# Kernel tuning notes

Measured on AMD Instinct MI355X. Metric: run time of the kernel, lower is better.

Reference implementation:

```python
import jax, jax.numpy as jnp
import numpy as np

T = 256          # n_tokens
APR = 3          # atoms_per_residue
N = T * APR      # n_atoms = 768
CA = 128         # atom_embedding_size
CP = 16          # atom_pair_embedding_size
CT = 384         # token_embedding_size
CS = 384         # single_embedding_size
CZ = 128         # pair_embedding_size
NB = 3           # num_block
H = 4            # num_head
DH = CA // H
NQ = 32          # num_queries (query block size)
NK = 128         # num_keys (local key window)


def _ln(x, g, b):
    m = jnp.mean(x, -1, keepdims=True)
    v = jnp.mean((x - m) ** 2, -1, keepdims=True)
    return (x - m) * jax.lax.rsqrt(v + 1e-5) * g + b


def setup_inputs() -> dict:
    key = jax.random.key(0)
    ks = jax.random.split(key, 32)
    w = lambda k, shape: jax.random.normal(k, shape, jnp.float32) * 0.02
    return {
        "ref_pos": jax.random.normal(ks[0], (N, 3), jnp.float32),
        "ref_space_uid": jax.random.randint(ks[1], (N,), 0, T),
        "r": jax.random.normal(ks[2], (N, 3), jnp.float32),
        "s": jax.random.normal(ks[3], (T, CS), jnp.float32),
        "z": jax.random.normal(ks[4], (T, T, CZ), jnp.float32),
        "W_pos": w(ks[5], (3, CA)),
        "W_pos_offset": w(ks[6], (3, CP)),
        "W_inv_sq_dist": w(ks[7], (1, CP)),
        "W_mask": w(ks[8], (1, CP)),
        "W_cond_a": w(ks[9], (CA, CP)),
        "W_cond_b": w(ks[10], (CA, CP)),
        "ln_s_g": jnp.ones((CS,), jnp.float32), "ln_s_b": jnp.zeros((CS,), jnp.float32),
        "W_single": w(ks[11], (CS, CA)),
        "ln_z_g": jnp.ones((CZ,), jnp.float32), "ln_z_b": jnp.zeros((CZ,), jnp.float32),
        "W_pair": w(ks[12], (CZ, CP)),
        "W_noisy": w(ks[13], (3, CA)),
        "W_mlp1": w(ks[14], (CP, CP)),
        "W_mlp2": w(ks[15], (CP, CP)),
        "W_mlp3": w(ks[16], (CP, CP)),
        "at_ln_g": jnp.ones((NB, CA), jnp.float32), "at_ln_b": jnp.zeros((NB, CA), jnp.float32),
        "at_Wq": w(ks[17], (NB, CA, CA)),
        "at_Wk": w(ks[18], (NB, CA, CA)),
        "at_Wv": w(ks[19], (NB, CA, CA)),
        "at_Wg": w(ks[20], (NB, CA, CA)),
        "at_lnp_g": jnp.ones((NB, CP), jnp.float32), "at_lnp_b": jnp.zeros((NB, CP), jnp.float32),
        "at_Wb": w(ks[21], (NB, CP, H)),
        "at_Wo": w(ks[22], (NB, CA, CA)),
        "at_ln2_g": jnp.ones((NB, CA), jnp.float32), "at_ln2_b": jnp.zeros((NB, CA), jnp.float32),
        "at_Wt1": w(ks[23], (NB, CA, 4 * CA)),
        "at_Wt2": w(ks[24], (NB, 4 * CA, CA)),
        "W_proj": w(ks[25], (CA, CT)),
    }


def _forward(ref_pos, ref_space_uid, r, s, z, W_pos, W_pos_offset, W_inv_sq_dist, W_mask,
             W_cond_a, W_cond_b, ln_s_g, ln_s_b, W_single, ln_z_g, ln_z_b, W_pair, W_noisy,
             W_mlp1, W_mlp2, W_mlp3, at_ln_g, at_ln_b, at_Wq, at_Wk, at_Wv, at_Wg,
             at_lnp_g, at_lnp_b, at_Wb, at_Wo, at_ln2_g, at_ln2_b, at_Wt1, at_Wt2, W_proj):
    c = ref_pos @ W_pos                                             # [N,CA]
    dist = ref_pos[:, None, :] - ref_pos[None, :, :]                # [N,N,3]
    maskf = (ref_space_uid[:, None] == ref_space_uid[None, :])[..., None].astype(jnp.float32)
    pair = (dist @ W_pos_offset) * maskf                            # [N,N,CP]
    sq = jnp.sum(dist * dist, -1, keepdims=True)                    # [N,N,1]
    pair = pair + ((1.0 / (1.0 + sq)) @ W_inv_sq_dist) * maskf
    pair = pair + (maskf @ W_mask) * maskf
    q = c
    # r is not None branch
    c = c + _ln(jnp.tile(s, (APR, 1)), ln_s_g, ln_s_b) @ W_single
    pair = pair + _ln(jnp.tile(z, (APR, APR, 1)), ln_z_g, ln_z_b) @ W_pair
    q = q + r @ W_noisy
    rc = jax.nn.relu(c)
    pair = pair + (rc @ W_cond_a)[:, None, :] + (rc @ W_cond_b)[None, :, :]
    h = jax.nn.relu(pair) @ W_mlp1
    h = jax.nn.relu(h) @ W_mlp2
    h = jax.nn.relu(h) @ W_mlp3
    pair = pair + h
    # sequence-local attention mask (AF3-style: query blocks of NQ attend a NK-wide window)
    idx = jnp.arange(N)
    center = (idx // NQ) * NQ + (NQ - 1) / 2.0
    beta = jnp.where(jnp.abs(idx[None, :].astype(jnp.float32) - center[:, None]) < NK / 2.0, 0.0, -1e9)
    scale = 1.0 / np.sqrt(DH).astype(np.float32)
    x = q
    for b in range(NB):
        a = _ln(x, at_ln_g[b], at_ln_b[b])
        qh = (a @ at_Wq[b]).reshape(N, H, DH)
        kh = (a @ at_Wk[b]).reshape(N, H, DH)
        vh = (a @ at_Wv[b]).reshape(N, H, DH)
        bias = _ln(pair, at_lnp_g[b], at_lnp_b[b]) @ at_Wb[b]       # [N,N,H]
        logits = jnp.einsum('ihd,jhd->hij', qh, kh) * scale + bias.transpose(2, 0, 1) + beta[None]
        attn = jax.nn.softmax(logits, axis=-1)
        o = jnp.einsum('hij,jhd->ihd', attn, vh)
        g = jax.nn.sigmoid(a @ at_Wg[b]).reshape(N, H, DH)
        x = x + (o * g).reshape(N, CA) @ at_Wo[b]
        t = _ln(x, at_ln2_g[b], at_ln2_b[b])
        x = x + jax.nn.relu(t @ at_Wt1[b]) @ at_Wt2[b]
    qout = jax.nn.relu(x @ W_proj)                                  # [N,CT]
    a_out = jnp.mean(qout.reshape(T, APR, CT), axis=-2)             # [T,CT]
    return a_out, qout, c, pair


def reference(ref_pos, ref_space_uid, r, s, z, W_pos, W_pos_offset, W_inv_sq_dist, W_mask,
              W_cond_a, W_cond_b, ln_s_g, ln_s_b, W_single, ln_z_g, ln_z_b, W_pair, W_noisy,
              W_mlp1, W_mlp2, W_mlp3, at_ln_g, at_ln_b, at_Wq, at_Wk, at_Wv, at_Wg,
              at_lnp_g, at_lnp_b, at_Wb, at_Wo, at_ln2_g, at_ln2_b, at_Wt1, at_Wt2, W_proj):
    return _forward(ref_pos, ref_space_uid, r, s, z, W_pos, W_pos_offset, W_inv_sq_dist, W_mask,
                    W_cond_a, W_cond_b, ln_s_g, ln_s_b, W_single, ln_z_g, ln_z_b, W_pair, W_noisy,
                    W_mlp1, W_mlp2, W_mlp3, at_ln_g, at_ln_b, at_Wq, at_Wk, at_Wv, at_Wg,
                    at_lnp_g, at_lnp_b, at_Wb, at_Wo, at_ln2_g, at_ln2_b, at_Wt1, at_Wt2, W_proj)
```

## Files before the change

kernel.cpp:

```cpp
#include <hip/hip_runtime.h>
#include <math.h>


__device__ __forceinline__ float sigmoidf_(float v) { return 1.f / (1.f + __expf(-v)); }

typedef __attribute__((ext_vector_type(4))) short s16x4;
typedef __attribute__((ext_vector_type(8))) short s16x8;
typedef __attribute__((ext_vector_type(4))) float f32x4;

__device__ __forceinline__ unsigned bfpack(float a, float b) {
  return (__float_as_uint(a) >> 16) | (__float_as_uint(b) & 0xFFFF0000u);
}
__device__ __forceinline__ short bf1(float a) { return (short)(__float_as_uint(a) >> 16); }

__global__ __launch_bounds__(256) void k_front(
    const float* __restrict__ z, const float* __restrict__ zg,
    const float* __restrict__ zlb, const float* __restrict__ W_pair,
    float* __restrict__ zp,
    const float* __restrict__ s, const float* __restrict__ g,
    const float* __restrict__ b, const float* __restrict__ W_single,
    const float* __restrict__ ref_pos, const float* __restrict__ r,
    const float* __restrict__ W_pos, const float* __restrict__ W_noisy,
    const float* __restrict__ Wca, const float* __restrict__ Wcb,
    float* __restrict__ c_out, float* __restrict__ x,
    float* __restrict__ ca, float* __restrict__ cb) {
  __shared__ __align__(128) float sm[5392];
  int t = threadIdx.x;
  int bid = blockIdx.x;
  if (bid < 1024) {
    float* bcp = sm + 5120;
    float* Bc = sm + 5376;
    {
      int ch = t & 15, kseg = t >> 4;
      float a = 0.f;
#pragma unroll
      for (int e = 0; e < 8; e++) {
        int k = kseg * 8 + e;
        a += zlb[k] * W_pair[k * 16 + ch];
      }
      bcp[kseg * 16 + ch] = a;
    }
    __syncthreads();
    if (t < 16) {
      float a = 0.f;
#pragma unroll
      for (int kseg = 0; kseg < 16; kseg++) a += bcp[kseg * 16 + t];
      Bc[t] = a;
    }
    __syncthreads();
    int w = t >> 6, l = t & 63;
    int kb = l & 15, rg = l >> 4;
    int row0 = bid * 64 + w * 16;
    char* stgw = (char*)(sm + w * 1280);
    float4 za[4], zb[4];
    float m_[4], rs_[4];
#pragma unroll
    for (int rr = 0; rr < 4; rr++) {
      long base = (long)(row0 + rg * 4 + rr) * 128 + kb * 8;
      za[rr] = *(const float4*)&z[base];
      zb[rr] = *(const float4*)&z[base + 4];
      float ps = za[rr].x + za[rr].y + za[rr].z + za[rr].w +
                 zb[rr].x + zb[rr].y + zb[rr].z + zb[rr].w;
      float pq = za[rr].x * za[rr].x + za[rr].y * za[rr].y + za[rr].z * za[rr].z +
                 za[rr].w * za[rr].w + zb[rr].x * zb[rr].x + zb[rr].y * zb[rr].y +
                 zb[rr].z * zb[rr].z + zb[rr].w * zb[rr].w;
#pragma unroll
      for (int o = 1; o < 16; o <<= 1) { ps += __shfl_xor(ps, o); pq += __shfl_xor(pq, o); }
      m_[rr] = ps * (1.f / 128.f);
      rs_[rr] = rsqrtf(pq * (1.f / 128.f) - m_[rr] * m_[rr] + 1e-5f);
    }
    {
      int kc = kb >> 1;
      int cbase = (kb & 1) * 8;
#pragma unroll
      for (int e = 0; e < 8; e++) {
        float a0 = ((e < 4 ? (&za[0].x)[e] : (&zb[0].x)[e - 4]) - m_[0]) * rs_[0];
        float a1 = ((e < 4 ? (&za[1].x)[e] : (&zb[1].x)[e - 4]) - m_[1]) * rs_[1];
        float a2 = ((e < 4 ? (&za[2].x)[e] : (&zb[2].x)[e - 4]) - m_[2]) * rs_[2];
        float a3 = ((e < 4 ? (&za[3].x)[e] : (&zb[3].x)[e - 4]) - m_[3]) * rs_[3];
        char* wp = stgw + kc * 640 + (cbase + e) * 32 + rg * 8;
        *(uint2*)wp = make_uint2(bfpack(a0, a1), bfpack(a2, a3));
      }
    }
    int c = l & 15;
    s16x8 bw[8];
#pragma unroll
    for (int kc = 0; kc < 8; kc++) {
      short e0, e1, e2, e3;
      {
        int kk = kc * 16 + 4 * rg;
        e0 = bf1(zg[kk] * W_pair[kk * 16 + c]);
        e1 = bf1(zg[kk + 1] * W_pair[(kk + 1) * 16 + c]);
        e2 = bf1(zg[kk + 2] * W_pair[(kk + 2) * 16 + c]);
        e3 = bf1(zg[kk + 3] * W_pair[(kk + 3) * 16 + c]);
      }
      bw[kc] = s16x8{e0, e1, e2, e3, (short)0, (short)0, (short)0, (short)0};
    }
    unsigned sbase = (unsigned)(uintptr_t)stgw;
    f32x4 acc = {0.f, 0.f, 0.f, 0.f};
#pragma unroll
    for (int kc = 0; kc < 8; kc++) {
      unsigned ra = sbase + (unsigned)(kc * 640 + c * 8 + rg * 128);
      s16x4 tr;
      asm volatile("s_waitcnt lgkmcnt(0)\n\tds_read_b64_tr_b16 %0, %1\n\ts_waitcnt lgkmcnt(0)"
                   : "=v"(tr) : "v"(ra) : "memory");
      s16x8 a8 = {tr[0], tr[1], tr[2], tr[3], (short)0, (short)0, (short)0, (short)0};
      acc = __builtin_amdgcn_mfma_f32_16x16x32_bf16(a8, bw[kc], acc, 0, 0, 0);
    }
    float bc = Bc[c];
#pragma unroll
    for (int rr = 0; rr < 4; rr++) {
      int row = row0 + rg * 4 + rr;
      zp[(long)row * 16 + c] = acc[rr] + bc;
    }
  } else {
    int tok = bid - 1024;
    float* sln = sm;
    float* ws = sm + 384;
    float* red = sm + 4480;
    float* rc = sm + 4488;
    float v0 = 0.f, v1 = 0.f, v2 = 0.f;
    if (t < 128) {
      v0 = s[tok * 384 + t]; v1 = s[tok * 384 + 128 + t]; v2 = s[tok * 384 + 256 + t];
      float ps = v0 + v1 + v2, pq = v0 * v0 + v1 * v1 + v2 * v2;
#pragma unroll
      for (int o = 1; o < 64; o <<= 1) { ps += __shfl_xor(ps, o); pq += __shfl_xor(pq, o); }
      if ((t & 63) == 0) { red[t >> 6] = ps; red[2 + (t >> 6)] = pq; }
    }
    __syncthreads();
    float ctv = 0.f;
    if (t < 128) {
      float mean = (red[0] + red[1]) * (1.f / 384.f);
      float var = (red[2] + red[3]) * (1.f / 384.f) - mean * mean;
      float rstd = rsqrtf(var + 1e-5f);
      sln[t] = (v0 - mean) * rstd * g[t] + b[t];
      sln[128 + t] = (v1 - mean) * rstd * g[128 + t] + b[128 + t];
      sln[256 + t] = (v2 - mean) * rstd * g[256 + t] + b[256 + t];
    }
    for (int c0 = 0; c0 < 384; c0 += 32) {
      __syncthreads();
#pragma unroll
      for (int m = 0; m < 4; m++) {
        int idx = (t + 256 * m) * 4;
        *(float4*)&ws[idx] = *(const float4*)&W_single[c0 * 128 + idx];
      }
      __syncthreads();
      if (t < 128) {
#pragma unroll 8
        for (int kk = 0; kk < 32; kk++) ctv += sln[c0 + kk] * ws[kk * 128 + t];
      }
    }
    float wp0 = 0.f, wp1 = 0.f, wp2 = 0.f, wn0 = 0.f, wn1 = 0.f, wn2 = 0.f;
    if (t < 128) {
      wp0 = W_pos[t]; wp1 = W_pos[128 + t]; wp2 = W_pos[256 + t];
      wn0 = W_noisy[t]; wn1 = W_noisy[128 + t]; wn2 = W_noisy[256 + t];
    }
#pragma unroll
    for (int a = 0; a < 3; a++) {
      int i = tok + 256 * a;
      float cc = 0.f;
      if (t < 128) {
        float p0 = ref_pos[i * 3], p1 = ref_pos[i * 3 + 1], p2 = ref_pos[i * 3 + 2];
        float r0 = r[i * 3], r1 = r[i * 3 + 1], r2 = r[i * 3 + 2];
        float c0 = p0 * wp0 + p1 * wp1 + p2 * wp2;
        x[i * 128 + t] = c0 + r0 * wn0 + r1 * wn1 + r2 * wn2;
        cc = c0 + ctv;
        c_out[i * 128 + t] = cc;
      }
      __syncthreads();
      if (t < 128) rc[t] = fmaxf(cc, 0.f);
      __syncthreads();
      if (t < 128) {
        int out_id = t >> 2, q = t & 3;
        const float* Wm = (out_id < 16) ? Wca : Wcb;
        int ch = out_id & 15;
        float acc = 0.f;
#pragma unroll
        for (int kk = 0; kk < 32; kk++) { int k = q * 32 + kk; acc += rc[k] * Wm[k * 16 + ch]; }
        acc += __shfl_xor(acc, 1);
        acc += __shfl_xor(acc, 2);
        if (q == 0) { if (out_id < 16) ca[i * 16 + ch] = acc; else cb[i * 16 + ch] = acc; }
      }
    }
  }
}

__global__ __launch_bounds__(256) void k_pairq(
    const float* __restrict__ ref_pos, const int* __restrict__ uid,
    const float* __restrict__ Wpo, const float* __restrict__ Wisd,
    const float* __restrict__ Wmask, const float* __restrict__ W1,
    const float* __restrict__ W2, const float* __restrict__ W3,
    const float* __restrict__ zp, const float* __restrict__ ca,
    const float* __restrict__ cb, const float* __restrict__ lnp_g,
    const float* __restrict__ lnp_b, const float* __restrict__ Wb,
    float* __restrict__ pair_out, float* __restrict__ biasA,
    const float* __restrict__ x, const float* __restrict__ lng,
    const float* __restrict__ lnb, const float* __restrict__ Wq,
    const float* __restrict__ Wk, const float* __restrict__ Wv,
    const float* __restrict__ Wg, float* __restrict__ qkvg) {
  __shared__ float jsx[256], jsy[256], jsz[256];
  __shared__ int jsu[256];
  __shared__ __align__(128) short stg[4][1280];
  __shared__ __align__(16) float pfs[4][1056];
  __shared__ float wgb[192];
  __shared__ float kbs[12];
  int t = threadIdx.x;
  int bid = blockIdx.x;
  if (bid >= 2304) {
    int r0 = (bid - 2304) * 2;
    float* asr_ = jsx;
    float* red_ = jsy;
    int row = t >> 7, c = t & 127;
    float xv = x[(r0 + row) * 128 + c];
    {
      float ps = xv, pq = xv * xv;
#pragma unroll
      for (int o = 1; o < 64; o <<= 1) { ps += __shfl_xor(ps, o); pq += __shfl_xor(pq, o); }
      int wv = t >> 6;
      if ((t & 63) == 0) { red_[wv] = ps; red_[4 + wv] = pq; }
      __syncthreads();
      float mean = (red_[2 * row] + red_[2 * row + 1]) * (1.f / 128.f);
      float var = (red_[4 + 2 * row] + red_[4 + 2 * row + 1]) * (1.f / 128.f) - mean * mean;
      float rstd = rsqrtf(var + 1e-5f);
      asr_[row * 128 + c] = (xv - mean) * rstd * lng[c] + lnb[c];
    }
    __syncthreads();
    {
      int c4 = (t & 127) * 4, row2 = t >> 7;
      int mtx = c4 >> 7, lc = c4 & 127;
      const float* Wm = (mtx == 0) ? Wq : (mtx == 1) ? Wk : (mtx == 2) ? Wv : Wg;
      float a0 = 0.f, a1 = 0.f, a2 = 0.f, a3 = 0.f;
#pragma unroll 8
      for (int k = 0; k < 128; k++) {
        float4 w = *(const float4*)&Wm[k * 128 + lc];
        float av = asr_[row2 * 128 + k];
        a0 += av * w.x; a1 += av * w.y; a2 += av * w.z; a3 += av * w.w;
      }
      *(float4*)&qkvg[(r0 + row2) * 512 + c4] = make_float4(a0, a1, a2, a3);
    }
    return;
  }
  int i = bid / 3, jb = bid % 3;
  int jg = jb * 256 + t;
  jsx[t] = ref_pos[jg * 3];
  jsy[t] = ref_pos[jg * 3 + 1];
  jsz[t] = ref_pos[jg * 3 + 2];
  jsu[t] = uid[jg];
  if (t >= 64) {
    int e = t - 64;
    if (e < 192) {
      int bq = e >> 6, k = (e >> 2) & 15, h = e & 3;
      wgb[e] = lnp_g[bq * 16 + k] * Wb[bq * 64 + k * 4 + h];
    }
  }
  if (t >= 48 && t < 60) {
    int e = t - 48, bq = e >> 2, h = e & 3;
    float a = 0.f;
#pragma unroll
    for (int cc = 0; cc < 16; cc++) a += lnp_b[bq * 16 + cc] * Wb[bq * 64 + cc * 4 + h];
    kbs[e] = a;
  }
  int w = t >> 6, l = t & 63;
  int c = l & 15, gr = l >> 4;
  float pix = ref_pos[i * 3], piy = ref_pos[i * 3 + 1], piz = ref_pos[i * 3 + 2];
  int ui = uid[i];
  float w0c = Wpo[c], w1c = Wpo[16 + c], w2c = Wpo[32 + c];
  float wic = Wisd[c], wmc = Wmask[c], cac = ca[i * 16 + c];
  s16x8 bw0 = {bf1(W1[(4 * gr + 0) * 16 + c]), bf1(W1[(4 * gr + 1) * 16 + c]),
               bf1(W1[(4 * gr + 2) * 16 + c]), bf1(W1[(4 * gr + 3) * 16 + c]),
               (short)0, (short)0, (short)0, (short)0};
  s16x8 bw1 = {bf1(W2[(4 * gr + 0) * 16 + c]), bf1(W2[(4 * gr + 1) * 16 + c]),
               bf1(W2[(4 * gr + 2) * 16 + c]), bf1(W2[(4 * gr + 3) * 16 + c]),
               (short)0, (short)0, (short)0, (short)0};
  s16x8 bw2 = {bf1(W3[(4 * gr + 0) * 16 + c]), bf1(W3[(4 * gr + 1) * 16 + c]),
               bf1(W3[(4 * gr + 2) * 16 + c]), bf1(W3[(4 * gr + 3) * 16 + c]),
               (short)0, (short)0, (short)0, (short)0};
  __syncthreads();
  char* sb = (char*)&stg[w][0];
  unsigned sbase = (unsigned)(uintptr_t)sb;
  f32x4 z4 = {0.f, 0.f, 0.f, 0.f};
#pragma unroll
  for (int g = 0; g < 4; g++) {
    float p0_, p1_, p2_, p3_;
    {
      int jl0 = w * 64 + g * 16 + 4 * gr;
#pragma unroll
      for (int r = 0; r < 4; r++) {
        int jloc = jl0 + r;
        int j = jb * 256 + jloc;
        float d0 = pix - jsx[jloc], d1 = piy - jsy[jloc], d2 = piz - jsz[jloc];
        float mk = (ui == jsu[jloc]) ? 1.f : 0.f;
        float inv = 1.f / (1.f + d0 * d0 + d1 * d1 + d2 * d2);
        float zv = zp[((long)((i & 255) << 8) + jloc) * 16 + c];
        float cbv = cb[j * 16 + c];
        float pv = mk * (d0 * w0c + d1 * w1c + d2 * w2c + inv * wic + wmc) + zv + cbv + cac;
        if (r == 0) p0_ = pv; else if (r == 1) p1_ = pv; else if (r == 2) p2_ = pv; else p3_ = pv;
      }
    }
    char* wp = sb + g * 640 + c * 32 + gr * 8;
    unsigned ra = sbase + (unsigned)(g * 640 + c * 8 + gr * 128);
    *(uint2*)wp = make_uint2(bfpack(fmaxf(p0_, 0.f), fmaxf(p1_, 0.f)),
                             bfpack(fmaxf(p2_, 0.f), fmaxf(p3_, 0.f)));
    s16x4 tr0;
    asm volatile("s_waitcnt lgkmcnt(0)\n\tds_read_b64_tr_b16 %0, %1\n\ts_waitcnt lgkmcnt(0)"
                 : "=v"(tr0) : "v"(ra) : "memory");
    s16x8 a8 = {tr0[0], tr0[1], tr0[2], tr0[3], (short)0, (short)0, (short)0, (short)0};
    f32x4 h1 = __builtin_amdgcn_mfma_f32_16x16x32_bf16(a8, bw0, z4, 0, 0, 0);
    *(uint2*)wp = make_uint2(bfpack(fmaxf(h1[0], 0.f), fmaxf(h1[1], 0.f)),
                             bfpack(fmaxf(h1[2], 0.f), fmaxf(h1[3], 0.f)));
    s16x4 tr1;
    asm volatile("s_waitcnt lgkmcnt(0)\n\tds_read_b64_tr_b16 %0, %1\n\ts_waitcnt lgkmcnt(0)"
                 : "=v"(tr1) : "v"(ra) : "memory");
    s16x8 a8b = {tr1[0], tr1[1], tr1[2], tr1[3], (short)0, (short)0, (short)0, (short)0};
    f32x4 h2 = __builtin_amdgcn_mfma_f32_16x16x32_bf16(a8b, bw1, z4, 0, 0, 0);
    *(uint2*)wp = make_uint2(bfpack(fmaxf(h2[0], 0.f), fmaxf(h2[1], 0.f)),
                             bfpack(fmaxf(h2[2], 0.f), fmaxf(h2[3], 0.f)));
    s16x4 tr2;
    asm volatile("s_waitcnt lgkmcnt(0)\n\tds_read_b64_tr_b16 %0, %1\n\ts_waitcnt lgkmcnt(0)"
                 : "=v"(tr2) : "v"(ra) : "memory");
    s16x8 a8c = {tr2[0], tr2[1], tr2[2], tr2[3], (short)0, (short)0, (short)0, (short)0};
    f32x4 h3 = __builtin_amdgcn_mfma_f32_16x16x32_bf16(a8c, bw2, z4, 0, 0, 0);
    float f0 = p0_ + h3[0], f1 = p1_ + h3[1], f2 = p2_ + h3[2], f3 = p3_ + h3[3];
    {
      int jl0 = w * 64 + g * 16 + 4 * gr;
      long pb = ((long)i * 768 + (long)(jb * 256 + jl0)) * 16 + c;
      pair_out[pb] = f0;
      pair_out[pb + 16] = f1;
      pair_out[pb + 32] = f2;
      pair_out[pb + 48] = f3;
    }
    *(float4*)&pfs[w][g * 264 + c * 16 + 4 * gr] = make_float4(f0, f1, f2, f3);
  }
  asm volatile("s_waitcnt lgkmcnt(0)" ::: "memory");
  int qb = i >> 5;
  int j = jb * 256 + t;
  unsigned jw = (unsigned)(j - (qb * 32 - 48));
  if (jw < 128u) {
    int gt = (t >> 4) & 3, jr = t & 15;
    float v[16];
#pragma unroll
    for (int cc = 0; cc < 16; cc++) v[cc] = pfs[w][gt * 264 + cc * 16 + jr];
    float m = 0.f;
#pragma unroll
    for (int cc = 0; cc < 16; cc++) m += v[cc];
    m *= (1.f / 16.f);
    float vv = 0.f;
#pragma unroll
    for (int cc = 0; cc < 16; cc++) { float d = v[cc] - m; vv += d * d; }
    float rs = rsqrtf(vv * (1.f / 16.f) + 1e-5f);
    float nrm[16];
#pragma unroll
    for (int cc = 0; cc < 16; cc++) nrm[cc] = (v[cc] - m) * rs;
    int qi = i & 31;
#pragma unroll
    for (int bq = 0; bq < 3; bq++) {
      float o0 = kbs[bq * 4 + 0], o1 = kbs[bq * 4 + 1];
      float o2 = kbs[bq * 4 + 2], o3 = kbs[bq * 4 + 3];
#pragma unroll
      for (int k = 0; k < 16; k++) {
        float nv = nrm[k];
        float4 wv = *(float4*)&wgb[bq * 64 + k * 4];
        o0 += nv * wv.x; o1 += nv * wv.y; o2 += nv * wv.z; o3 += nv * wv.w;
      }
      long base = (long)(bq * 96 + qb * 4) * 4096 + (long)qi * 128 + jw;
      biasA[base] = o0;
      biasA[base + 4096] = o1;
      biasA[base + 2 * 4096] = o2;
      biasA[base + 3 * 4096] = o3;
    }
  }
}

__global__ __launch_bounds__(256) void k_attn2(
    const float* __restrict__ qkvg, const float* __restrict__ biasb,
    float* __restrict__ og) {
  int qt = blockIdx.x >> 2, h = blockIdx.x & 3, t = threadIdx.x;
  int i0 = qt * 16;
  int qb32 = qt >> 1;
  int lo = qb32 * 32 - 48;
  int qoff = (qt & 1) * 16;
  __shared__ float qs[16][36];
  __shared__ float ks[128][36];
  __shared__ float vs[128][36];
  __shared__ float L[16][132];
  {
    int e = t * 8;
    int qi = e >> 7, k8 = e & 127;
    const float* bb = &biasb[(long)(qb32 * 4 + h) * 4096 + (long)(qoff + qi) * 128];
#pragma unroll
    for (int m = 0; m < 2; m++) {
      int k4 = k8 + m * 4;
      int j4 = lo + k4;
      float4 bv;
      if (j4 >= 0 && j4 <= 764) bv = *(const float4*)&bb[k4];
      else bv = make_float4(-1e30f, -1e30f, -1e30f, -1e30f);
      *(float4*)&L[qi][k4] = bv;
    }
  }
  if (t < 128) {
    int qi = t >> 3, dq = (t & 7) * 4;
    *(float4*)&qs[qi][dq] = *(const float4*)&qkvg[(i0 + qi) * 512 + h * 32 + dq];
  }
  {
    int kj = t >> 1, dh = (t & 1) * 16;
    int j = lo + kj;
    if (j >= 0 && j < 768) {
      const float4* sk = (const float4*)&qkvg[j * 512 + 128 + h * 32 + dh];
      const float4* sv = (const float4*)&qkvg[j * 512 + 256 + h * 32 + dh];
#pragma unroll
      for (int m = 0; m < 4; m++) {
        *(float4*)&ks[kj][dh + 4 * m] = sk[m];
        *(float4*)&vs[kj][dh + 4 * m] = sv[m];
      }
    } else {
      float4 zz = {0, 0, 0, 0};
#pragma unroll
      for (int m = 0; m < 4; m++) {
        *(float4*)&ks[kj][dh + 4 * m] = zz;
        *(float4*)&vs[kj][dh + 4 * m] = zz;
      }
    }
  }
  __syncthreads();
  const float scale = 0.17677669529663687f;
  {
    int qi = t & 15, kb = t >> 4;
    float4 qr[8];
#pragma unroll
    for (int m = 0; m < 8; m++) qr[m] = *(float4*)&qs[qi][m * 4];
#pragma unroll
    for (int kk = 0; kk < 8; kk++) {
      int kj = kb * 8 + kk;
      float acc = 0.f;
#pragma unroll
      for (int m = 0; m < 8; m++) {
        float4 kv = *(float4*)&ks[kj][m * 4];
        acc += qr[m].x * kv.x + qr[m].y * kv.y + qr[m].z * kv.z + qr[m].w * kv.w;
      }
      L[qi][kj] += acc * scale;
    }
  }
  __syncthreads();
  int qi = t >> 4, sg = t & 15;
  float mx = -1e30f;
#pragma unroll
  for (int k2 = 0; k2 < 8; k2++) mx = fmaxf(mx, L[qi][sg * 8 + k2]);
#pragma unroll
  for (int o = 1; o < 16; o <<= 1) mx = fmaxf(mx, __shfl_xor(mx, o));
  float sum = 0.f;
#pragma unroll
  for (int k2 = 0; k2 < 8; k2++) {
    int kj = sg * 8 + k2;
    float e = __expf(L[qi][kj] - mx);
    L[qi][kj] = e;
    sum += e;
  }
#pragma unroll
  for (int o = 1; o < 16; o <<= 1) sum += __shfl_xor(sum, o);
  float rden = 1.f / sum;
  __syncthreads();
  {
    int d2 = (t & 15) * 2;
    float a0 = 0.f, a1 = 0.f;
#pragma unroll 8
    for (int kj = 0; kj < 128; kj++) {
      float p = L[qi][kj];
      float2 v = *(float2*)&vs[kj][d2];
      a0 += p * v.x; a1 += p * v.y;
    }
    int i = i0 + qi;
    float2 gr = *(const float2*)&qkvg[i * 512 + 384 + h * 32 + d2];
    float2 o2;
    o2.x = a0 * rden * sigmoidf_(gr.x);
    o2.y = a1 * rden * sigmoidf_(gr.y);
    *(float2*)&og[i * 128 + h * 32 + d2] = o2;
  }
}

template <int MODE>
__global__ __launch_bounds__(512, 1) void k_fusedT(
    const float* __restrict__ og, const float* __restrict__ Wo,
    const float* __restrict__ g2, const float* __restrict__ b2,
    const float* __restrict__ Wt1, const float* __restrict__ Wt2,
    float* __restrict__ x,
    const float* __restrict__ lng_n, const float* __restrict__ lnb_n,
    const float* __restrict__ Wq, const float* __restrict__ Wk,
    const float* __restrict__ Wv, const float* __restrict__ Wg,
    float* __restrict__ qkvg, const float* __restrict__ W_proj,
    float* __restrict__ out) {
  int t = threadIdx.x;
  int r0 = blockIdx.x * 3;
  __shared__ float osr[3][128];
  __shared__ float xns[3][128];
  __shared__ float asr[3][128];
  __shared__ float hs[3][512];
  __shared__ float part[4][3][128];
  __shared__ float part2[4][3][512];
  __shared__ float red[12];
  if (t < 384) {
    int rr = t >> 7, c = t & 127;
    osr[rr][c] = og[(r0 + rr) * 128 + c];
    xns[rr][c] = x[(r0 + rr) * 128 + c];
  }
  __syncthreads();
  if (t < 384) {
    int c4 = (t & 31) * 4, row = (t >> 5) % 3, q = t / 96;
    int k0 = q * 32;
    float a0 = 0.f, a1 = 0.f, a2 = 0.f, a3 = 0.f;
#pragma unroll 8
    for (int kk = 0; kk < 32; kk++) {
      int k = k0 + kk;
      float4 w = *(const float4*)&Wo[k * 128 + c4];
      float av = osr[row][k];
      a0 += av * w.x; a1 += av * w.y; a2 += av * w.z; a3 += av * w.w;
    }
    *(float4*)&part[q][row][c4] = make_float4(a0, a1, a2, a3);
  }
  __syncthreads();
  if (t < 384) {
    int rr = t >> 7, c = t & 127;
    float xv = xns[rr][c] + part[0][rr][c] + part[1][rr][c] + part[2][rr][c] + part[3][rr][c];
    float ps = xv, pq = xv * xv;
#pragma unroll
    for (int o = 1; o < 64; o <<= 1) { ps += __shfl_xor(ps, o); pq += __shfl_xor(pq, o); }
    int wv = t >> 6;
    if ((t & 63) == 0) { red[wv] = ps; red[6 + wv] = pq; }
  }
  __syncthreads();
  if (t < 384) {
    int rr = t >> 7, c = t & 127;
    float xv = xns[rr][c] + part[0][rr][c] + part[1][rr][c] + part[2][rr][c] + part[3][rr][c];
    float mean = (red[2 * rr] + red[2 * rr + 1]) * (1.f / 128.f);
    float var = (red[6 + 2 * rr] + red[6 + 2 * rr + 1]) * (1.f / 128.f) - mean * mean;
    float rstd = rsqrtf(var + 1e-5f);
    xns[rr][c] = xv;
    asr[rr][c] = (xv - mean) * rstd * g2[c] + b2[c];
  }
  __syncthreads();
  {
    int cg4 = (t & 127) * 4, ks = t >> 7;
    int k0 = ks * 32;
    float a00 = 0.f, a01 = 0.f, a02 = 0.f, a03 = 0.f;
    float a10 = 0.f, a11 = 0.f, a12 = 0.f, a13 = 0.f;
    float a20 = 0.f, a21 = 0.f, a22 = 0.f, a23 = 0.f;
#pragma unroll 8
    for (int kk = 0; kk < 32; kk++) {
      int k = k0 + kk;
      float4 w = *(const float4*)&Wt1[k * 512 + cg4];
      float v0 = asr[0][k], v1 = asr[1][k], v2 = asr[2][k];
      a00 += v0 * w.x; a01 += v0 * w.y; a02 += v0 * w.z; a03 += v0 * w.w;
      a10 += v1 * w.x; a11 += v1 * w.y; a12 += v1 * w.z; a13 += v1 * w.w;
      a20 += v2 * w.x; a21 += v2 * w.y; a22 += v2 * w.z; a23 += v2 * w.w;
    }
    *(float4*)&part2[ks][0][cg4] = make_float4(a00, a01, a02, a03);
    *(float4*)&part2[ks][1][cg4] = make_float4(a10, a11, a12, a13);
    *(float4*)&part2[ks][2][cg4] = make_float4(a20, a21, a22, a23);
  }
  __syncthreads();
  {
#pragma unroll
    for (int row = 0; row < 3; row++) {
      float v = part2[0][row][t] + part2[1][row][t] + part2[2][row][t] + part2[3][row][t];
      hs[row][t] = fmaxf(v, 0.f);
    }
  }
  __syncthreads();
  {
    int cg4 = (t & 31) * 4, ks = t >> 5;
    int k0 = ks * 32;
    float a00 = 0.f, a01 = 0.f, a02 = 0.f, a03 = 0.f;
    float a10 = 0.f, a11 = 0.f, a12 = 0.f, a13 = 0.f;
    float a20 = 0.f, a21 = 0.f, a22 = 0.f, a23 = 0.f;
#pragma unroll 8
    for (int kk = 0; kk < 32; kk++) {
      int k = k0 + kk;
      float4 w = *(const float4*)&Wt2[k * 128 + cg4];
      float v0 = hs[0][k], v1 = hs[1][k], v2 = hs[2][k];
      a00 += v0 * w.x; a01 += v0 * w.y; a02 += v0 * w.z; a03 += v0 * w.w;
      a10 += v1 * w.x; a11 += v1 * w.y; a12 += v1 * w.z; a13 += v1 * w.w;
      a20 += v2 * w.x; a21 += v2 * w.y; a22 += v2 * w.z; a23 += v2 * w.w;
    }
    float* p3 = &part2[0][0][0];
    *(float4*)&p3[(ks * 3 + 0) * 128 + cg4] = make_float4(a00, a01, a02, a03);
    *(float4*)&p3[(ks * 3 + 1) * 128 + cg4] = make_float4(a10, a11, a12, a13);
    *(float4*)&p3[(ks * 3 + 2) * 128 + cg4] = make_float4(a20, a21, a22, a23);
  }
  __syncthreads();
  if (t < 384) {
    int rr = t >> 7, c = t & 127;
    const float* p3 = &part2[0][0][0];
    float acc = 0.f;
#pragma unroll
    for (int ks = 0; ks < 16; ks++) acc += p3[(ks * 3 + rr) * 128 + c];
    float xf = xns[rr][c] + acc;
    x[(r0 + rr) * 128 + c] = xf;
    xns[rr][c] = xf;
  }
  __syncthreads();
  if (MODE == 1) {
    if (t < 384) {
      int rr = t >> 7, c = t & 127;
      float xv = xns[rr][c];
      float ps = xv, pq = xv * xv;
#pragma unroll
      for (int o = 1; o < 64; o <<= 1) { ps += __shfl_xor(ps, o); pq += __shfl_xor(pq, o); }
      int wv = t >> 6;
      if ((t & 63) == 0) { red[wv] = ps; red[6 + wv] = pq; }
    }
    __syncthreads();
    if (t < 384) {
      int rr = t >> 7, c = t & 127;
      float xv = xns[rr][c];
      float mean = (red[2 * rr] + red[2 * rr + 1]) * (1.f / 128.f);
      float var = (red[6 + 2 * rr] + red[6 + 2 * rr + 1]) * (1.f / 128.f) - mean * mean;
      float rstd = rsqrtf(var + 1e-5f);
      asr[rr][c] = (xv - mean) * rstd * lng_n[c] + lnb_n[c];
    }
    __syncthreads();
    {
      int cg4 = (t & 127) * 4, ks = t >> 7;
      int k0 = ks * 32;
      int mtx = cg4 >> 7, lc = cg4 & 127;
      const float* Wm = (mtx == 0) ? Wq : (mtx == 1) ? Wk : (mtx == 2) ? Wv : Wg;
      float a00 = 0.f, a01 = 0.f, a02 = 0.f, a03 = 0.f;
      float a10 = 0.f, a11 = 0.f, a12 = 0.f, a13 = 0.f;
      float a20 = 0.f, a21 = 0.f, a22 = 0.f, a23 = 0.f;
#pragma unroll 8
      for (int kk = 0; kk < 32; kk++) {
        int k = k0 + kk;
        float4 w = *(const float4*)&Wm[k * 128 + lc];
        float v0 = asr[0][k], v1 = asr[1][k], v2 = asr[2][k];
        a00 += v0 * w.x; a01 += v0 * w.y; a02 += v0 * w.z; a03 += v0 * w.w;
        a10 += v1 * w.x; a11 += v1 * w.y; a12 += v1 * w.z; a13 += v1 * w.w;
        a20 += v2 * w.x; a21 += v2 * w.y; a22 += v2 * w.z; a23 += v2 * w.w;
      }
      *(float4*)&part2[ks][0][cg4] = make_float4(a00, a01, a02, a03);
      *(float4*)&part2[ks][1][cg4] = make_float4(a10, a11, a12, a13);
      *(float4*)&part2[ks][2][cg4] = make_float4(a20, a21, a22, a23);
    }
    __syncthreads();
    {
#pragma unroll
      for (int row = 0; row < 3; row++) {
        float v = part2[0][row][t] + part2[1][row][t] + part2[2][row][t] + part2[3][row][t];
        qkvg[(r0 + row) * 512 + t] = v;
      }
    }
  }
  if (MODE == 2) {
    if (t < 384) {
      int tk = blockIdx.x;
      float a0 = 0.f, a1 = 0.f, a2 = 0.f;
#pragma unroll 8
      for (int k = 0; k < 128; k++) {
        float w = W_proj[k * 384 + t];
        a0 += xns[0][k] * w; a1 += xns[1][k] * w; a2 += xns[2][k] * w;
      }
      a0 = fmaxf(a0, 0.f); a1 = fmaxf(a1, 0.f); a2 = fmaxf(a2, 0.f);
      out[98304 + (tk * 3 + 0) * 384 + t] = a0;
      out[98304 + (tk * 3 + 1) * 384 + t] = a1;
      out[98304 + (tk * 3 + 2) * 384 + t] = a2;
      out[tk * 384 + t] = (a0 + a1 + a2) * (1.f / 3.f);
    }
  }
}

extern "C" void kernel_launch(void* const* d_in, const int* in_sizes, int n_in,
                              void* d_out, int out_size, void* d_ws, size_t ws_size,
                              hipStream_t stream) {
  const float* ref_pos  = (const float*)d_in[0];
  const int*   uid      = (const int*)d_in[1];
  const float* r        = (const float*)d_in[2];
  const float* s        = (const float*)d_in[3];
  const float* z        = (const float*)d_in[4];
  const float* W_pos    = (const float*)d_in[5];
  const float* Wpo      = (const float*)d_in[6];
  const float* Wisd     = (const float*)d_in[7];
  const float* Wmask    = (const float*)d_in[8];
  const float* Wca      = (const float*)d_in[9];
  const float* Wcb      = (const float*)d_in[10];
  const float* ln_s_g   = (const float*)d_in[11];
  const float* ln_s_b   = (const float*)d_in[12];
  const float* W_single = (const float*)d_in[13];
  const float* ln_z_g   = (const float*)d_in[14];
  const float* ln_z_b   = (const float*)d_in[15];
  const float* W_pair   = (const float*)d_in[16];
  const float* W_noisy  = (const float*)d_in[17];
  const float* W_mlp1   = (const float*)d_in[18];
  const float* W_mlp2   = (const float*)d_in[19];
  const float* W_mlp3   = (const float*)d_in[20];
  const float* at_ln_g  = (const float*)d_in[21];
  const float* at_ln_b  = (const float*)d_in[22];
  const float* at_Wq    = (const float*)d_in[23];
  const float* at_Wk    = (const float*)d_in[24];
  const float* at_Wv    = (const float*)d_in[25];
  const float* at_Wg    = (const float*)d_in[26];
  const float* at_lnp_g = (const float*)d_in[27];
  const float* at_lnp_b = (const float*)d_in[28];
  const float* at_Wb    = (const float*)d_in[29];
  const float* at_Wo    = (const float*)d_in[30];
  const float* at_ln2_g = (const float*)d_in[31];
  const float* at_ln2_b = (const float*)d_in[32];
  const float* at_Wt1   = (const float*)d_in[33];
  const float* at_Wt2   = (const float*)d_in[34];
  const float* W_proj   = (const float*)d_in[35];
  float* out = (float*)d_out;
  float* W = (float*)d_ws;
  float* x     = W;
  float* ca    = W + 98304;
  float* cb    = W + 110592;
  float* zp    = W + 122880;
  float* biasA = W + 1171456;
  float* qkvg  = W + 2351104;
  float* og    = W + 2744320;

  k_front<<<1280, 256, 0, stream>>>(z, ln_z_g, ln_z_b, W_pair, zp,
                                    s, ln_s_g, ln_s_b, W_single, ref_pos, r,
                                    W_pos, W_noisy, Wca, Wcb,
                                    out + 393216, x, ca, cb);
  k_pairq<<<2688, 256, 0, stream>>>(ref_pos, uid, Wpo, Wisd, Wmask, W_mlp1, W_mlp2,
                                    W_mlp3, zp, ca, cb, at_lnp_g, at_lnp_b, at_Wb,
                                    out + 491520, biasA,
                                    x, at_ln_g, at_ln_b, at_Wq, at_Wk, at_Wv, at_Wg,
                                    qkvg);
  k_attn2<<<192, 256, 0, stream>>>(qkvg, biasA, og);
  k_fusedT<1><<<256, 512, 0, stream>>>(og, at_Wo, at_ln2_g, at_ln2_b, at_Wt1, at_Wt2, x,
                                       at_ln_g + 128, at_ln_b + 128,
                                       at_Wq + 16384, at_Wk + 16384,
                                       at_Wv + 16384, at_Wg + 16384, qkvg,
                                       nullptr, nullptr);
  k_attn2<<<192, 256, 0, stream>>>(qkvg, biasA + 393216, og);
  k_fusedT<1><<<256, 512, 0, stream>>>(og, at_Wo + 16384, at_ln2_g + 128, at_ln2_b + 128,
                                       at_Wt1 + 65536, at_Wt2 + 65536, x,
                                       at_ln_g + 256, at_ln_b + 256,
                                       at_Wq + 32768, at_Wk + 32768,
                                       at_Wv + 32768, at_Wg + 32768, qkvg,
                                       nullptr, nullptr);
  k_attn2<<<192, 256, 0, stream>>>(qkvg, biasA + 786432, og);
  k_fusedT<2><<<256, 512, 0, stream>>>(og, at_Wo + 32768, at_ln2_g + 256, at_ln2_b + 256,
                                       at_Wt1 + 131072, at_Wt2 + 131072, x,
                                       nullptr, nullptr, nullptr, nullptr,
                                       nullptr, nullptr, nullptr, W_proj, out);
}
```

Before: 143.7 us.

## Fuse local attention into transition kernel and ping-pong qkvg buffers

Removes the separate k_attn2 launches and computes attention for each block's 3 query rows inside k_fusedT, reading K/V straight from global memory. Because a block now reads other rows' qkvg while other blocks write the next block's qkvg, the code alternates between two qkvg buffers. This saves three kernel launches and the og round trip through global memory. In exchange it adds a serial per-row loop with several block barriers, and K/V values are re-read from global/L2 by every block instead of being shared through LDS across 16 queries.

Measured after the change: 186.7 us. +29.9%, slower.

```diff
diff --git a/kernel.cpp b/kernel.cpp
--- a/kernel.cpp
+++ b/kernel.cpp
@@ -371,122 +371,17 @@
   }
 }
 
-__global__ __launch_bounds__(256) void k_attn2(
-    const float* __restrict__ qkvg, const float* __restrict__ biasb,
-    float* __restrict__ og) {
-  int qt = blockIdx.x >> 2, h = blockIdx.x & 3, t = threadIdx.x;
-  int i0 = qt * 16;
-  int qb32 = qt >> 1;
-  int lo = qb32 * 32 - 48;
-  int qoff = (qt & 1) * 16;
-  __shared__ float qs[16][36];
-  __shared__ float ks[128][36];
-  __shared__ float vs[128][36];
-  __shared__ float L[16][132];
-  {
-    int e = t * 8;
-    int qi = e >> 7, k8 = e & 127;
-    const float* bb = &biasb[(long)(qb32 * 4 + h) * 4096 + (long)(qoff + qi) * 128];
-#pragma unroll
-    for (int m = 0; m < 2; m++) {
-      int k4 = k8 + m * 4;
-      int j4 = lo + k4;
-      float4 bv;
-      if (j4 >= 0 && j4 <= 764) bv = *(const float4*)&bb[k4];
-      else bv = make_float4(-1e30f, -1e30f, -1e30f, -1e30f);
-      *(float4*)&L[qi][k4] = bv;
-    }
-  }
-  if (t < 128) {
-    int qi = t >> 3, dq = (t & 7) * 4;
-    *(float4*)&qs[qi][dq] = *(const float4*)&qkvg[(i0 + qi) * 512 + h * 32 + dq];
-  }
-  {
-    int kj = t >> 1, dh = (t & 1) * 16;
-    int j = lo + kj;
-    if (j >= 0 && j < 768) {
-      const float4* sk = (const float4*)&qkvg[j * 512 + 128 + h * 32 + dh];
-      const float4* sv = (const float4*)&qkvg[j * 512 + 256 + h * 32 + dh];
-#pragma unroll
-      for (int m = 0; m < 4; m++) {
-        *(float4*)&ks[kj][dh + 4 * m] = sk[m];
-        *(float4*)&vs[kj][dh + 4 * m] = sv[m];
-      }
-    } else {
-      float4 zz = {0, 0, 0, 0};
-#pragma unroll
-      for (int m = 0; m < 4; m++) {
-        *(float4*)&ks[kj][dh + 4 * m] = zz;
-        *(float4*)&vs[kj][dh + 4 * m] = zz;
-      }
-    }
-  }
-  __syncthreads();
-  const float scale = 0.17677669529663687f;
-  {
-    int qi = t & 15, kb = t >> 4;
-    float4 qr[8];
-#pragma unroll
-    for (int m = 0; m < 8; m++) qr[m] = *(float4*)&qs[qi][m * 4];
-#pragma unroll
-    for (int kk = 0; kk < 8; kk++) {
-      int kj = kb * 8 + kk;
-      float acc = 0.f;
-#pragma unroll
-      for (int m = 0; m < 8; m++) {
-        float4 kv = *(float4*)&ks[kj][m * 4];
-        acc += qr[m].x * kv.x + qr[m].y * kv.y + qr[m].z * kv.z + qr[m].w * kv.w;
-      }
-      L[qi][kj] += acc * scale;
-    }
-  }
-  __syncthreads();
-  int qi = t >> 4, sg = t & 15;
-  float mx = -1e30f;
-#pragma unroll
-  for (int k2 = 0; k2 < 8; k2++) mx = fmaxf(mx, L[qi][sg * 8 + k2]);
-#pragma unroll
-  for (int o = 1; o < 16; o <<= 1) mx = fmaxf(mx, __shfl_xor(mx, o));
-  float sum = 0.f;
-#pragma unroll
-  for (int k2 = 0; k2 < 8; k2++) {
-    int kj = sg * 8 + k2;
-    float e = __expf(L[qi][kj] - mx);
-    L[qi][kj] = e;
-    sum += e;
-  }
-#pragma unroll
-  for (int o = 1; o < 16; o <<= 1) sum += __shfl_xor(sum, o);
-  float rden = 1.f / sum;
-  __syncthreads();
-  {
-    int d2 = (t & 15) * 2;
-    float a0 = 0.f, a1 = 0.f;
-#pragma unroll 8
-    for (int kj = 0; kj < 128; kj++) {
-      float p = L[qi][kj];
-      float2 v = *(float2*)&vs[kj][d2];
-      a0 += p * v.x; a1 += p * v.y;
-    }
-    int i = i0 + qi;
-    float2 gr = *(const float2*)&qkvg[i * 512 + 384 + h * 32 + d2];
-    float2 o2;
-    o2.x = a0 * rden * sigmoidf_(gr.x);
-    o2.y = a1 * rden * sigmoidf_(gr.y);
-    *(float2*)&og[i * 128 + h * 32 + d2] = o2;
-  }
-}
-
 template <int MODE>
 __global__ __launch_bounds__(512, 1) void k_fusedT(
-    const float* __restrict__ og, const float* __restrict__ Wo,
+    const float* __restrict__ qkvg_in, const float* __restrict__ biasb,
+    const float* __restrict__ Wo,
     const float* __restrict__ g2, const float* __restrict__ b2,
     const float* __restrict__ Wt1, const float* __restrict__ Wt2,
     float* __restrict__ x,
     const float* __restrict__ lng_n, const float* __restrict__ lnb_n,
     const float* __restrict__ Wq, const float* __restrict__ Wk,
     const float* __restrict__ Wv, const float* __restrict__ Wg,
-    float* __restrict__ qkvg, const float* __restrict__ W_proj,
+    float* __restrict__ qkvg_out, const float* __restrict__ W_proj,
     float* __restrict__ out) {
   int t = threadIdx.x;
   int r0 = blockIdx.x * 3;
@@ -497,9 +392,65 @@
   __shared__ float part[4][3][128];
   __shared__ float part2[4][3][512];
   __shared__ float red[12];
+  __shared__ float qs2[128];
+  __shared__ float Ls[4 * 132];
+  __shared__ float redp[16];
+  const float scale = 0.17677669529663687f;
+  for (int rr2 = 0; rr2 < 3; rr2++) {
+    int i = r0 + rr2;
+    int qb32 = i >> 5, qi5 = i & 31, lo = qb32 * 32 - 48;
+    if (t < 128) qs2[t] = qkvg_in[i * 512 + t];
+    __syncthreads();
+    int h = t >> 7, kj = t & 127;
+    int j = lo + kj;
+    float v = -1e30f;
+    if (j >= 0 && j < 768) {
+      const float4* kp = (const float4*)&qkvg_in[j * 512 + 128 + h * 32];
+      float acc = 0.f;
+#pragma unroll
+      for (int m4 = 0; m4 < 8; m4++) {
+        float4 kv = kp[m4];
+        float4 qv = *(float4*)&qs2[h * 32 + m4 * 4];
+        acc += qv.x * kv.x + qv.y * kv.y + qv.z * kv.z + qv.w * kv.w;
+      }
+      v = acc * scale + biasb[(qb32 * 4 + h) * 4096 + qi5 * 128 + kj];
+    }
+    float mx = v;
+#pragma unroll
+    for (int o = 1; o < 64; o <<= 1) mx = fmaxf(mx, __shfl_xor(mx, o));
+    int wv = t >> 6;
+    if ((t & 63) == 0) redp[wv] = mx;
+    __syncthreads();
+    float m = fmaxf(redp[2 * h], redp[2 * h + 1]);
+    float e = __expf(v - m);
+    float sm = e;
+#pragma unroll
+    for (int o = 1; o < 64; o <<= 1) sm += __shfl_xor(sm, o);
+    if ((t & 63) == 0) redp[8 + wv] = sm;
+    __syncthreads();
+    float S = redp[8 + 2 * h] + redp[8 + 2 * h + 1];
+    Ls[h * 132 + kj] = e / S;
+    __syncthreads();
+    {
+      int h3 = t >> 7, d = (t >> 2) & 31, q2 = t & 3;
+      float acc = 0.f;
+#pragma unroll 8
+      for (int kk = 0; kk < 32; kk++) {
+        int kjj = q2 * 32 + kk;
+        long jj = (long)(lo + kjj);
+        acc += Ls[h3 * 132 + kjj] * qkvg_in[jj * 512 + 256 + h3 * 32 + d];
+      }
+      acc += __shfl_xor(acc, 1);
+      acc += __shfl_xor(acc, 2);
+      if (q2 == 0) {
+        float gg = qkvg_in[i * 512 + 384 + h3 * 32 + d];
+        osr[rr2][h3 * 32 + d] = acc * sigmoidf_(gg);
+      }
+    }
+    __syncthreads();
+  }
   if (t < 384) {
     int rr = t >> 7, c = t & 127;
-    osr[rr][c] = og[(r0 + rr) * 128 + c];
     xns[rr][c] = x[(r0 + rr) * 128 + c];
   }
   __syncthreads();
@@ -643,7 +594,7 @@
 #pragma unroll
       for (int row = 0; row < 3; row++) {
         float v = part2[0][row][t] + part2[1][row][t] + part2[2][row][t] + part2[3][row][t];
-        qkvg[(r0 + row) * 512 + t] = v;
+        qkvg_out[(r0 + row) * 512 + t] = v;
       }
     }
   }
@@ -706,13 +657,13 @@
   const float* W_proj   = (const float*)d_in[35];
   float* out = (float*)d_out;
   float* W = (float*)d_ws;
-  float* x     = W;
-  float* ca    = W + 98304;
-  float* cb    = W + 110592;
-  float* zp    = W + 122880;
-  float* biasA = W + 1171456;
-  float* qkvg  = W + 2351104;
-  float* og    = W + 2744320;
+  float* x      = W;
+  float* ca     = W + 98304;
+  float* cb     = W + 110592;
+  float* zp     = W + 122880;
+  float* biasA  = W + 1171456;
+  float* qkvgA  = W + 2351104;
+  float* qkvgB  = W + 2744320;
 
   k_front<<<1280, 256, 0, stream>>>(z, ln_z_g, ln_z_b, W_pair, zp,
                                     s, ln_s_g, ln_s_b, W_single, ref_pos, r,
@@ -722,22 +673,22 @@
                                     W_mlp3, zp, ca, cb, at_lnp_g, at_lnp_b, at_Wb,
                                     out + 491520, biasA,
                                     x, at_ln_g, at_ln_b, at_Wq, at_Wk, at_Wv, at_Wg,
-                                    qkvg);
-  k_attn2<<<192, 256, 0, stream>>>(qkvg, biasA, og);
-  k_fusedT<1><<<256, 512, 0, stream>>>(og, at_Wo, at_ln2_g, at_ln2_b, at_Wt1, at_Wt2, x,
+                                    qkvgA);
+  k_fusedT<1><<<256, 512, 0, stream>>>(qkvgA, biasA, at_Wo, at_ln2_g, at_ln2_b,
+                                       at_Wt1, at_Wt2, x,
                                        at_ln_g + 128, at_ln_b + 128,
                                        at_Wq + 16384, at_Wk + 16384,
-                                       at_Wv + 16384, at_Wg + 16384, qkvg,
+                                       at_Wv + 16384, at_Wg + 16384, qkvgB,
                                        nullptr, nullptr);
-  k_attn2<<<192, 256, 0, stream>>>(qkvg, biasA + 393216, og);
-  k_fusedT<1><<<256, 512, 0, stream>>>(og, at_Wo + 16384, at_ln2_g + 128, at_ln2_b + 128,
+  k_fusedT<1><<<256, 512, 0, stream>>>(qkvgB, biasA + 393216, at_Wo + 16384,
+                                       at_ln2_g + 128, at_ln2_b + 128,
                                        at_Wt1 + 65536, at_Wt2 + 65536, x,
                                        at_ln_g + 256, at_ln_b + 256,
                                        at_Wq + 32768, at_Wk + 32768,
-                                       at_Wv + 32768, at_Wg + 32768, qkvg,
+                                       at_Wv + 32768, at_Wg + 32768, qkvgA,
                                        nullptr, nullptr);
-  k_attn2<<<192, 256, 0, stream>>>(qkvg, biasA + 786432, og);
-  k_fusedT<2><<<256, 512, 0, stream>>>(og, at_Wo + 32768, at_ln2_g + 256, at_ln2_b + 256,
+  k_fusedT<2><<<256, 512, 0, stream>>>(qkvgA, biasA + 786432, at_Wo + 32768,
+                                       at_ln2_g + 256, at_ln2_b + 256,
                                        at_Wt1 + 131072, at_Wt2 + 131072, x,
                                        nullptr, nullptr, nullptr, nullptr,
                                        nullptr, nullptr, nullptr, W_proj, out);
```
